# Kernel tuning notes

Hardware: AMD Instinct MI355X
Metric: run time of the kernel (lower is better)

The kernel has to match this reference:

```python
import jax, jax.numpy as jnp
import numpy as np

NEG_SLOPE = 0.01  # torch nn.LeakyReLU default


def setup_inputs() -> dict:
    key = jax.random.key(0)
    ks = jax.random.split(key, 6)
    B, L, C, D = 4, 1024, 128, 64
    return {
        "queries": jax.random.normal(ks[0], (B, L, C), dtype=jnp.float32),
        "keys": jax.random.normal(ks[1], (B, L, C), dtype=jnp.float32),
        "values": jax.random.normal(ks[2], (B, L, C), dtype=jnp.float32),
        "linear_l": jax.random.normal(ks[3], (C, D), dtype=jnp.float32) * 0.05,
        "linear_r": jax.random.normal(ks[4], (C, D), dtype=jnp.float32) * 0.05,
        "a": jax.random.normal(ks[5], (D, 1), dtype=jnp.float32) * 0.05,
    }


def reference(queries, keys, values, linear_l, linear_r, a):
    # keys/values are accepted by the torch forward but unused in its math.
    # g_l, g_r: (B, L, D)
    g_l = jnp.einsum('blc,cd->bld', queries, linear_l)
    g_r = jnp.einsum('blc,cd->bld', queries, linear_r)
    # torch repeat/repeat_interleave + view(b,l,l,-1) yields
    # g_sum[b, x, y] = g_l[b, y] + g_r[b, x]  -> (B, L, L, D)
    g_sum = g_l[:, None, :, :] + g_r[:, :, None, :]
    g_sum = jnp.where(g_sum >= 0, g_sum, NEG_SLOPE * g_sum)  # LeakyReLU
    e = jnp.einsum('bxyd,d->bxy', g_sum, a[:, 0])            # (B, L, L)
    scores = jax.nn.softmax(e, axis=-1)                       # dropout is identity in eval
    y = jnp.einsum('bxy,byd->bxd', scores, g_r)               # (B, L, D)
    return (y, scores)
```

## Files before the change

### kernel.cpp

```cpp
#include <hip/hip_runtime.h>
#include <math.h>

#define LL   1024
#define NROW 4096
#define DD   64
#define CC   128

#define C1H 0.505f
#define C2H 0.495f

typedef short    bf16x8 __attribute__((ext_vector_type(8)));
typedef float    f32x4  __attribute__((ext_vector_type(4)));
typedef _Float16 hf2    __attribute__((ext_vector_type(2)));

static __device__ __forceinline__ unsigned short bf16rne(float f) {
  unsigned u = __float_as_uint(f);
  u += 0x7fffu + ((u >> 16) & 1u);
  return (unsigned short)(u >> 16);
}

static __device__ __forceinline__ unsigned rflu(unsigned v) {
  return __builtin_amdgcn_readfirstlane(v);
}
static __device__ __forceinline__ float rflf(float v) {
  return __uint_as_float(__builtin_amdgcn_readfirstlane(__float_as_uint(v)));
}

static __device__ __forceinline__ void unpkf16(unsigned u, float& lo, float& hi) {
  union { unsigned u; hf2 h; } v; v.u = u;
  lo = (float)v.h.x;
  hi = (float)v.h.y;
}

__global__ __launch_bounds__(256) void k_proj(
    const float* __restrict__ q, const float* __restrict__ Wl,
    const float* __restrict__ Wr, const float* __restrict__ a,
    uint4* __restrict__ glg, _Float16* __restrict__ gr16,
    unsigned short* __restrict__ grTf,
    float* __restrict__ AL, float* __restrict__ AR) {
  const int bl0 = blockIdx.x * 8;
  const int b = bl0 >> 10;
  const int t = threadIdx.x;
  __shared__ __align__(16) float qs[8 * CC];
  __shared__ __align__(16) unsigned short trT[DD][8];
  __shared__ __align__(16) _Float16 trL[8][DD];

  ((float4*)qs)[t] = ((const float4*)(q + (size_t)bl0 * CC))[t];
  __syncthreads();

  const int rr = t >> 6;
  const int d  = t & 63;
  const int r0 = rr * 2, r1 = rr * 2 + 1;
  const float* q0 = qs + r0 * CC;
  const float* q1 = qs + r1 * CC;

  float aL0 = 0, aL1 = 0, aR0 = 0, aR1 = 0;
  float bL0 = 0, bL1 = 0, bR0 = 0, bR1 = 0;
#pragma unroll 8
  for (int c = 0; c < CC; c += 2) {
    float wl0 = Wl[c * DD + d],       wr0 = Wr[c * DD + d];
    float wl1 = Wl[(c + 1) * DD + d], wr1 = Wr[(c + 1) * DD + d];
    aL0 = fmaf(q0[c], wl0, aL0);  bL0 = fmaf(q0[c + 1], wl1, bL0);
    aL1 = fmaf(q1[c], wl0, aL1);  bL1 = fmaf(q1[c + 1], wl1, bL1);
    aR0 = fmaf(q0[c], wr0, aR0);  bR0 = fmaf(q0[c + 1], wr1, bR0);
    aR1 = fmaf(q1[c], wr0, aR1);  bR1 = fmaf(q1[c + 1], wr1, bR1);
  }
  float gL0 = aL0 + bL0, gL1 = aL1 + bL1;
  float gR0 = aR0 + bR0, gR1 = aR1 + bR1;

  trL[r0][d] = (_Float16)gL0;
  trL[r1][d] = (_Float16)gL1;
  gr16[(size_t)(bl0 + r0) * DD + d] = (_Float16)gR0;
  gr16[(size_t)(bl0 + r1) * DD + d] = (_Float16)gR1;
  trT[d][r0] = bf16rne(gR0);
  trT[d][r1] = bf16rne(gR1);

  float av = a[d];
  float vL0 = av * gL0, vL1 = av * gL1, vR0 = av * gR0, vR1 = av * gR1;
#pragma unroll
  for (int off = 1; off < 64; off <<= 1) {
    vL0 += __shfl_xor(vL0, off, 64);
    vL1 += __shfl_xor(vL1, off, 64);
    vR0 += __shfl_xor(vR0, off, 64);
    vR1 += __shfl_xor(vR1, off, 64);
  }
  if (d == 0) {
    AL[bl0 + r0] = vL0; AL[bl0 + r1] = vL1;
    AR[bl0 + r0] = vR0; AR[bl0 + r1] = vR1;
  }
  __syncthreads();
  if (t < 64) {
    const int kc = (bl0 & 1023) >> 5;
    const int hi = ((bl0 & 1023) >> 3) & 3;
    ((uint4*)grTf)[((size_t)((b * 32 + kc) * 4 + (t >> 4)) << 6) +
                   hi * 16 + (t & 15)] = *(const uint4*)&trT[t][0];
  } else if (t < 128) {
    int tt = t - 64;
    int r = tt >> 3, g = tt & 7;
    glg[(((size_t)(b * 8 + g)) << 10) + (bl0 & 1023) + r] =
        *(const uint4*)&trL[r][g * 8];
  }
}

__global__ __launch_bounds__(512, 4) void k_fused(
    const uint4* __restrict__ glg, const _Float16* __restrict__ gr16,
    const unsigned short* __restrict__ grTf,
    const float* __restrict__ AL, const float* __restrict__ AR,
    const float* __restrict__ a,
    float* __restrict__ scores, float* __restrict__ yout) {
  const int bl0 = blockIdx.x * 8;
  const int b = bl0 >> 10;
  const int t = threadIdx.x;
  const int w = t >> 6, l = t & 63;

  __shared__ __align__(16) float grL32[8 * DD];
  __shared__ __align__(16) unsigned short eb[8704];
  __shared__ __align__(16) float sPV[8][4][8][17];
  __shared__ __align__(16) float sSx[8][8];

  uint4 gv[4][2][2];
#pragma unroll
  for (int dblk = 0; dblk < 4; ++dblk)
#pragma unroll
    for (int yc = 0; yc < 2; ++yc)
#pragma unroll
      for (int g2 = 0; g2 < 2; ++g2)
        gv[dblk][yc][g2] =
            glg[(((size_t)(b * 8 + dblk * 2 + g2)) << 10) + yc * 512 + t];

  if (t < 256) {
    unsigned u = ((const unsigned*)(gr16 + (size_t)bl0 * DD))[t];
    float lo, hi;
    unpkf16(u, lo, hi);
    grL32[t * 2]     = lo;
    grL32[t * 2 + 1] = hi;
  }

  float sa[64];
#pragma unroll
  for (int k = 0; k < 16; ++k) {
    float4 av = *(const float4*)&a[k * 4];
    sa[k * 4 + 0] = rflf(av.x);
    sa[k * 4 + 1] = rflf(av.y);
    sa[k * 4 + 2] = rflf(av.z);
    sa[k * 4 + 3] = rflf(av.w);
  }

  float pr[8];
#pragma unroll
  for (int x = 0; x < 8; ++x) pr[x] = C1H * rflf(AR[bl0 + x]);

  float alv[2];
  alv[0] = AL[b * LL + t];
  alv[1] = AL[b * LL + 512 + t];

  float pacc[8][2];
#pragma unroll
  for (int x = 0; x < 8; ++x) { pacc[x][0] = 0.f; pacc[x][1] = 0.f; }

  __syncthreads();

  const float4* grL4 = (const float4*)grL32;
#pragma unroll
  for (int dblk = 0; dblk < 4; ++dblk) {
    float gl32[2][16];
#pragma unroll
    for (int yc = 0; yc < 2; ++yc) {
      unpkf16(gv[dblk][yc][0].x, gl32[yc][0],  gl32[yc][1]);
      unpkf16(gv[dblk][yc][0].y, gl32[yc][2],  gl32[yc][3]);
      unpkf16(gv[dblk][yc][0].z, gl32[yc][4],  gl32[yc][5]);
      unpkf16(gv[dblk][yc][0].w, gl32[yc][6],  gl32[yc][7]);
      unpkf16(gv[dblk][yc][1].x, gl32[yc][8],  gl32[yc][9]);
      unpkf16(gv[dblk][yc][1].y, gl32[yc][10], gl32[yc][11]);
      unpkf16(gv[dblk][yc][1].z, gl32[yc][12], gl32[yc][13]);
      unpkf16(gv[dblk][yc][1].w, gl32[yc][14], gl32[yc][15]);
    }
#pragma unroll
    for (int x = 0; x < 8; ++x) {
      float4 g0 = grL4[x * 16 + dblk * 4 + 0];
      float4 g1 = grL4[x * 16 + dblk * 4 + 1];
      float4 g2 = grL4[x * 16 + dblk * 4 + 2];
      float4 g3 = grL4[x * 16 + dblk * 4 + 3];
#pragma unroll
      for (int yc = 0; yc < 2; ++yc) {
        const float* gl = gl32[yc];
        float s = pacc[x][yc];
        s = fmaf(fabsf(gl[0]  + g0.x), sa[dblk * 16 + 0],  s);
        s = fmaf(fabsf(gl[1]  + g0.y), sa[dblk * 16 + 1],  s);
        s = fmaf(fabsf(gl[2]  + g0.z), sa[dblk * 16 + 2],  s);
        s = fmaf(fabsf(gl[3]  + g0.w), sa[dblk * 16 + 3],  s);
        s = fmaf(fabsf(gl[4]  + g1.x), sa[dblk * 16 + 4],  s);
        s = fmaf(fabsf(gl[5]  + g1.y), sa[dblk * 16 + 5],  s);
        s = fmaf(fabsf(gl[6]  + g1.z), sa[dblk * 16 + 6],  s);
        s = fmaf(fabsf(gl[7]  + g1.w), sa[dblk * 16 + 7],  s);
        s = fmaf(fabsf(gl[8]  + g2.x), sa[dblk * 16 + 8],  s);
        s = fmaf(fabsf(gl[9]  + g2.y), sa[dblk * 16 + 9],  s);
        s = fmaf(fabsf(gl[10] + g2.z), sa[dblk * 16 + 10], s);
        s = fmaf(fabsf(gl[11] + g2.w), sa[dblk * 16 + 11], s);
        s = fmaf(fabsf(gl[12] + g3.x), sa[dblk * 16 + 12], s);
        s = fmaf(fabsf(gl[13] + g3.y), sa[dblk * 16 + 13], s);
        s = fmaf(fabsf(gl[14] + g3.z), sa[dblk * 16 + 14], s);
        s = fmaf(fabsf(gl[15] + g3.w), sa[dblk * 16 + 15], s);
        pacc[x][yc] = s;
      }
    }
  }

  float ev[8][2], lsum[8];
#pragma unroll
  for (int x = 0; x < 8; ++x) {
    ev[x][0] = __expf(fmaf(C2H, pacc[x][0], pr[x] + C1H * alv[0]));
    ev[x][1] = __expf(fmaf(C2H, pacc[x][1], pr[x] + C1H * alv[1]));
    lsum[x] = ev[x][0] + ev[x][1];
  }
#pragma unroll
  for (int off = 1; off < 64; off <<= 1) {
#pragma unroll
    for (int x = 0; x < 8; ++x) lsum[x] += __shfl_xor(lsum[x], off, 64);
  }
  if (l == 0) {
#pragma unroll
    for (int x = 0; x < 8; ++x) sSx[x][w] = lsum[x];
  }
  __syncthreads();

  float isv[8];
#pragma unroll
  for (int x = 0; x < 8; ++x) {
    float4 s0 = *(const float4*)&sSx[x][0];
    float4 s1 = *(const float4*)&sSx[x][4];
    isv[x] = 1.0f / (((s0.x + s0.y) + (s0.z + s0.w)) +
                     ((s1.x + s1.y) + (s1.z + s1.w)));
  }

  float pv_[8][2];
#pragma unroll
  for (int yc = 0; yc < 2; ++yc) {
    int y = yc * 512 + t;
    int kc = y >> 5, k32 = t & 31;
#pragma unroll
    for (int x = 0; x < 8; ++x) {
      float p = ev[x][yc] * isv[x];
      pv_[x][yc] = p;
      eb[kc * 256 + x * 32 + k32] = bf16rne(p);
    }
  }
  __syncthreads();

  f32x4 acc[4] = {{0.f, 0.f, 0.f, 0.f}, {0.f, 0.f, 0.f, 0.f},
                  {0.f, 0.f, 0.f, 0.f}, {0.f, 0.f, 0.f, 0.f}};
  const int row16 = l & 15, hh = l >> 4;
#pragma unroll
  for (int kk = 0; kk < 4; ++kk) {
    int kc = w * 4 + kk;
    bf16x8 af = *(const bf16x8*)&eb[kc * 256 + row16 * 32 + hh * 8];
#pragma unroll
    for (int nt = 0; nt < 4; ++nt) {
      bf16x8 bfv = *(const bf16x8*)(grTf +
          ((((size_t)((b * 32 + kc) * 4 + nt)) << 6) + l) * 8);
      acc[nt] = __builtin_amdgcn_mfma_f32_16x16x32_bf16(af, bfv, acc[nt], 0, 0, 0);
    }
  }
  if (l < 32) {
#pragma unroll
    for (int nt = 0; nt < 4; ++nt)
#pragma unroll
      for (int i = 0; i < 4; ++i)
        sPV[w][nt][hh * 4 + i][row16] = acc[nt][i];
  }
  __syncthreads();
  {
    int x = t >> 6, dcol = t & 63, nt = dcol >> 4, col = dcol & 15;
    float r = 0.f;
#pragma unroll
    for (int ww = 0; ww < 8; ++ww) r += sPV[ww][nt][x][col];
    yout[(size_t)(bl0 + x) * DD + dcol] = r;
  }

#pragma unroll
  for (int yc = 0; yc < 2; ++yc) {
    int y = yc * 512 + t;
#pragma unroll
    for (int x = 0; x < 8; ++x)
      __builtin_nontemporal_store(pv_[x][yc],
                                  &scores[((size_t)(bl0 + x) << 10) + y]);
  }
}

extern "C" void kernel_launch(void* const* d_in, const int* in_sizes, int n_in,
                              void* d_out, int out_size, void* d_ws, size_t ws_size,
                              hipStream_t stream) {
  const float* q  = (const float*)d_in[0];
  const float* Wl = (const float*)d_in[3];
  const float* Wr = (const float*)d_in[4];
  const float* a  = (const float*)d_in[5];

  float* yout = (float*)d_out;
  float* esc  = yout + NROW * DD;

  float* ws = (float*)d_ws;
  float* AL = ws;
  float* AR = AL + NROW;
  uint4* glg = (uint4*)(AR + NROW);
  _Float16* gr16 = (_Float16*)(glg + (size_t)NROW * 8);
  unsigned short* grTf = (unsigned short*)(gr16 + (size_t)NROW * DD);

  k_proj <<<NROW / 8, 256, 0, stream>>>(q, Wl, Wr, a, glg, gr16, grTf, AL, AR);
  k_fused<<<NROW / 8, 512, 0, stream>>>(glg, gr16, grTf, AL, AR, a, esc, yout);
}
```

Baseline: 32.77 us.

## Halve fused kernel block size, give each thread four key columns

The fused scores kernel now runs 256 threads per block instead of 512. Each thread handles four key columns instead of two, and each wave does eight MFMA k-chunks instead of four. The gl loads move from a prefetch at kernel start into the per-d-block loop, and the score stores are issued as soon as the probabilities are computed, so the pv_ register array goes away. This amortises the broadcast loads of the query-row data and the softmax reduction over more work per thread, and halves the cross-wave partial sums. In exchange it uses more registers per thread, has fewer waves to hide latency, and loses the early load prefetch.

```diff
diff --git a/kernel.cpp b/kernel.cpp
--- a/kernel.cpp
+++ b/kernel.cpp
@@ -19,9 +19,6 @@
   return (unsigned short)(u >> 16);
 }
 
-static __device__ __forceinline__ unsigned rflu(unsigned v) {
-  return __builtin_amdgcn_readfirstlane(v);
-}
 static __device__ __forceinline__ float rflf(float v) {
   return __uint_as_float(__builtin_amdgcn_readfirstlane(__float_as_uint(v)));
 }
@@ -102,7 +99,7 @@
   }
 }
 
-__global__ __launch_bounds__(512, 4) void k_fused(
+__global__ __launch_bounds__(256, 4) void k_fused(
     const uint4* __restrict__ glg, const _Float16* __restrict__ gr16,
     const unsigned short* __restrict__ grTf,
     const float* __restrict__ AL, const float* __restrict__ AR,
@@ -115,20 +112,10 @@
 
   __shared__ __align__(16) float grL32[8 * DD];
   __shared__ __align__(16) unsigned short eb[8704];
-  __shared__ __align__(16) float sPV[8][4][8][17];
-  __shared__ __align__(16) float sSx[8][8];
-
-  uint4 gv[4][2][2];
-#pragma unroll
-  for (int dblk = 0; dblk < 4; ++dblk)
-#pragma unroll
-    for (int yc = 0; yc < 2; ++yc)
-#pragma unroll
-      for (int g2 = 0; g2 < 2; ++g2)
-        gv[dblk][yc][g2] =
-            glg[(((size_t)(b * 8 + dblk * 2 + g2)) << 10) + yc * 512 + t];
-
-  if (t < 256) {
+  __shared__ __align__(16) float sPV[4][4][8][17];
+  __shared__ __align__(16) float sSx[8][4];
+
+  {
     unsigned u = ((const unsigned*)(gr16 + (size_t)bl0 * DD))[t];
     float lo, hi;
     unpkf16(u, lo, hi);
@@ -150,30 +137,34 @@
 #pragma unroll
   for (int x = 0; x < 8; ++x) pr[x] = C1H * rflf(AR[bl0 + x]);
 
-  float alv[2];
-  alv[0] = AL[b * LL + t];
-  alv[1] = AL[b * LL + 512 + t];
-
-  float pacc[8][2];
-#pragma unroll
-  for (int x = 0; x < 8; ++x) { pacc[x][0] = 0.f; pacc[x][1] = 0.f; }
+  float alv[4];
+#pragma unroll
+  for (int yc = 0; yc < 4; ++yc) alv[yc] = AL[b * LL + yc * 256 + t];
+
+  float pacc[8][4];
+#pragma unroll
+  for (int x = 0; x < 8; ++x)
+#pragma unroll
+    for (int yc = 0; yc < 4; ++yc) pacc[x][yc] = 0.f;
 
   __syncthreads();
 
   const float4* grL4 = (const float4*)grL32;
 #pragma unroll
   for (int dblk = 0; dblk < 4; ++dblk) {
-    float gl32[2][16];
-#pragma unroll
-    for (int yc = 0; yc < 2; ++yc) {
-      unpkf16(gv[dblk][yc][0].x, gl32[yc][0],  gl32[yc][1]);
-      unpkf16(gv[dblk][yc][0].y, gl32[yc][2],  gl32[yc][3]);
-      unpkf16(gv[dblk][yc][0].z, gl32[yc][4],  gl32[yc][5]);
-      unpkf16(gv[dblk][yc][0].w, gl32[yc][6],  gl32[yc][7]);
-      unpkf16(gv[dblk][yc][1].x, gl32[yc][8],  gl32[yc][9]);
-      unpkf16(gv[dblk][yc][1].y, gl32[yc][10], gl32[yc][11]);
-      unpkf16(gv[dblk][yc][1].z, gl32[yc][12], gl32[yc][13]);
-      unpkf16(gv[dblk][yc][1].w, gl32[yc][14], gl32[yc][15]);
+    float gl32[4][16];
+#pragma unroll
+    for (int yc = 0; yc < 4; ++yc) {
+      uint4 g0 = glg[(((size_t)(b * 8 + dblk * 2 + 0)) << 10) + yc * 256 + t];
+      uint4 g1 = glg[(((size_t)(b * 8 + dblk * 2 + 1)) << 10) + yc * 256 + t];
+      unpkf16(g0.x, gl32[yc][0],  gl32[yc][1]);
+      unpkf16(g0.y, gl32[yc][2],  gl32[yc][3]);
+      unpkf16(g0.z, gl32[yc][4],  gl32[yc][5]);
+      unpkf16(g0.w, gl32[yc][6],  gl32[yc][7]);
+      unpkf16(g1.x, gl32[yc][8],  gl32[yc][9]);
+      unpkf16(g1.y, gl32[yc][10], gl32[yc][11]);
+      unpkf16(g1.z, gl32[yc][12], gl32[yc][13]);
+      unpkf16(g1.w, gl32[yc][14], gl32[yc][15]);
     }
 #pragma unroll
     for (int x = 0; x < 8; ++x) {
@@ -182,7 +173,7 @@
       float4 g2 = grL4[x * 16 + dblk * 4 + 2];
       float4 g3 = grL4[x * 16 + dblk * 4 + 3];
 #pragma unroll
-      for (int yc = 0; yc < 2; ++yc) {
+      for (int yc = 0; yc < 4; ++yc) {
         const float* gl = gl32[yc];
         float s = pacc[x][yc];
         s = fmaf(fabsf(gl[0]  + g0.x), sa[dblk * 16 + 0],  s);
@@ -206,12 +197,15 @@
     }
   }
 
-  float ev[8][2], lsum[8];
+  float ev[8][4], lsum[8];
 #pragma unroll
   for (int x = 0; x < 8; ++x) {
-    ev[x][0] = __expf(fmaf(C2H, pacc[x][0], pr[x] + C1H * alv[0]));
-    ev[x][1] = __expf(fmaf(C2H, pacc[x][1], pr[x] + C1H * alv[1]));
-    lsum[x] = ev[x][0] + ev[x][1];
+    lsum[x] = 0.f;
+#pragma unroll
+    for (int yc = 0; yc < 4; ++yc) {
+      ev[x][yc] = __expf(fmaf(C2H, pacc[x][yc], pr[x] + C1H * alv[yc]));
+      lsum[x] += ev[x][yc];
+    }
   }
 #pragma unroll
   for (int off = 1; off < 64; off <<= 1) {
@@ -228,20 +222,17 @@
 #pragma unroll
   for (int x = 0; x < 8; ++x) {
     float4 s0 = *(const float4*)&sSx[x][0];
-    float4 s1 = *(const float4*)&sSx[x][4];
-    isv[x] = 1.0f / (((s0.x + s0.y) + (s0.z + s0.w)) +
-                     ((s1.x + s1.y) + (s1.z + s1.w)));
-  }
-
-  float pv_[8][2];
-#pragma unroll
-  for (int yc = 0; yc < 2; ++yc) {
-    int y = yc * 512 + t;
+    isv[x] = 1.0f / ((s0.x + s0.y) + (s0.z + s0.w));
+  }
+
+#pragma unroll
+  for (int yc = 0; yc < 4; ++yc) {
+    int y = yc * 256 + t;
     int kc = y >> 5, k32 = t & 31;
 #pragma unroll
     for (int x = 0; x < 8; ++x) {
       float p = ev[x][yc] * isv[x];
-      pv_[x][yc] = p;
+      __builtin_nontemporal_store(p, &scores[((size_t)(bl0 + x) << 10) + y]);
       eb[kc * 256 + x * 32 + k32] = bf16rne(p);
     }
   }
@@ -251,8 +242,8 @@
                   {0.f, 0.f, 0.f, 0.f}, {0.f, 0.f, 0.f, 0.f}};
   const int row16 = l & 15, hh = l >> 4;
 #pragma unroll
-  for (int kk = 0; kk < 4; ++kk) {
-    int kc = w * 4 + kk;
+  for (int kk = 0; kk < 8; ++kk) {
+    int kc = w * 8 + kk;
     bf16x8 af = *(const bf16x8*)&eb[kc * 256 + row16 * 32 + hh * 8];
 #pragma unroll
     for (int nt = 0; nt < 4; ++nt) {
@@ -269,21 +260,14 @@
         sPV[w][nt][hh * 4 + i][row16] = acc[nt][i];
   }
   __syncthreads();
-  {
-    int x = t >> 6, dcol = t & 63, nt = dcol >> 4, col = dcol & 15;
+#pragma unroll
+  for (int rep = 0; rep < 2; ++rep) {
+    int o = t + rep * 256;
+    int x = o >> 6, dcol = o & 63, nt = dcol >> 4, col = dcol & 15;
     float r = 0.f;
 #pragma unroll
-    for (int ww = 0; ww < 8; ++ww) r += sPV[ww][nt][x][col];
+    for (int ww = 0; ww < 4; ++ww) r += sPV[ww][nt][x][col];
     yout[(size_t)(bl0 + x) * DD + dcol] = r;
-  }
-
-#pragma unroll
-  for (int yc = 0; yc < 2; ++yc) {
-    int y = yc * 512 + t;
-#pragma unroll
-    for (int x = 0; x < 8; ++x)
-      __builtin_nontemporal_store(pv_[x][yc],
-                                  &scores[((size_t)(bl0 + x) << 10) + y]);
   }
 }
 
@@ -306,5 +290,5 @@
   unsigned short* grTf = (unsigned short*)(gr16 + (size_t)NROW * DD);
 
   k_proj <<<NROW / 8, 256, 0, stream>>>(q, Wl, Wr, a, glg, gr16, grTf, AL, AR);
-  k_fused<<<NROW / 8, 512, 0, stream>>>(glg, gr16, grTf, AL, AR, a, esc, yout);
-}
+  k_fused<<<NROW / 8, 256, 0, stream>>>(glg, gr16, grTf, AL, AR, a, esc, yout);
+}
```

New measurement: 36.78 us. 1.12x slower.

## Split fused softmax kernel into score kernel and separate PV matmul kernel

Applied to the files above, without the earlier changes.

The fused kernel is split in two. The first kernel computes the softmax scores, writes them to global memory and also stores a bf16 copy to a workspace buffer. The second kernel reads that buffer and runs the MFMA product with g_r to produce y. This drops the LDS staging buffer and a barrier from the scores kernel, which may raise occupancy. In exchange it adds an extra kernel launch and a global write plus read of about 8 MB of bf16 probabilities.

```diff
diff --git a/kernel.cpp b/kernel.cpp
--- a/kernel.cpp
+++ b/kernel.cpp
@@ -19,9 +19,6 @@
   return (unsigned short)(u >> 16);
 }
 
-static __device__ __forceinline__ unsigned rflu(unsigned v) {
-  return __builtin_amdgcn_readfirstlane(v);
-}
 static __device__ __forceinline__ float rflf(float v) {
   return __uint_as_float(__builtin_amdgcn_readfirstlane(__float_as_uint(v)));
 }
@@ -102,20 +99,17 @@
   }
 }
 
-__global__ __launch_bounds__(512, 4) void k_fused(
+__global__ __launch_bounds__(512, 4) void k_e(
     const uint4* __restrict__ glg, const _Float16* __restrict__ gr16,
-    const unsigned short* __restrict__ grTf,
     const float* __restrict__ AL, const float* __restrict__ AR,
     const float* __restrict__ a,
-    float* __restrict__ scores, float* __restrict__ yout) {
+    float* __restrict__ scores, unsigned short* __restrict__ ebg) {
   const int bl0 = blockIdx.x * 8;
   const int b = bl0 >> 10;
   const int t = threadIdx.x;
   const int w = t >> 6, l = t & 63;
 
   __shared__ __align__(16) float grL32[8 * DD];
-  __shared__ __align__(16) unsigned short eb[8704];
-  __shared__ __align__(16) float sPV[8][4][8][17];
   __shared__ __align__(16) float sSx[8][8];
 
   uint4 gv[4][2][2];
@@ -233,7 +227,7 @@
                      ((s1.x + s1.y) + (s1.z + s1.w)));
   }
 
-  float pv_[8][2];
+  const size_t eb0 = (size_t)blockIdx.x * 8192;
 #pragma unroll
   for (int yc = 0; yc < 2; ++yc) {
     int y = yc * 512 + t;
@@ -241,19 +235,31 @@
 #pragma unroll
     for (int x = 0; x < 8; ++x) {
       float p = ev[x][yc] * isv[x];
-      pv_[x][yc] = p;
-      eb[kc * 256 + x * 32 + k32] = bf16rne(p);
+      __builtin_nontemporal_store(p, &scores[((size_t)(bl0 + x) << 10) + y]);
+      __builtin_nontemporal_store(bf16rne(p), &ebg[eb0 + kc * 256 + x * 32 + k32]);
     }
   }
-  __syncthreads();
+}
+
+__global__ __launch_bounds__(512, 4) void k_pv(
+    const unsigned short* __restrict__ ebg,
+    const unsigned short* __restrict__ grTf,
+    float* __restrict__ yout) {
+  const int bl0 = blockIdx.x * 8;
+  const int b = bl0 >> 10;
+  const int t = threadIdx.x;
+  const int w = t >> 6, l = t & 63;
+
+  __shared__ __align__(16) float sPV[8][4][8][17];
 
   f32x4 acc[4] = {{0.f, 0.f, 0.f, 0.f}, {0.f, 0.f, 0.f, 0.f},
                   {0.f, 0.f, 0.f, 0.f}, {0.f, 0.f, 0.f, 0.f}};
   const int row16 = l & 15, hh = l >> 4;
+  const size_t eb0 = (size_t)blockIdx.x * 8192;
 #pragma unroll
   for (int kk = 0; kk < 4; ++kk) {
     int kc = w * 4 + kk;
-    bf16x8 af = *(const bf16x8*)&eb[kc * 256 + row16 * 32 + hh * 8];
+    bf16x8 af = *(const bf16x8*)&ebg[eb0 + kc * 256 + row16 * 32 + hh * 8];
 #pragma unroll
     for (int nt = 0; nt < 4; ++nt) {
       bf16x8 bfv = *(const bf16x8*)(grTf +
@@ -275,15 +281,6 @@
 #pragma unroll
     for (int ww = 0; ww < 8; ++ww) r += sPV[ww][nt][x][col];
     yout[(size_t)(bl0 + x) * DD + dcol] = r;
-  }
-
-#pragma unroll
-  for (int yc = 0; yc < 2; ++yc) {
-    int y = yc * 512 + t;
-#pragma unroll
-    for (int x = 0; x < 8; ++x)
-      __builtin_nontemporal_store(pv_[x][yc],
-                                  &scores[((size_t)(bl0 + x) << 10) + y]);
   }
 }
 
@@ -304,7 +301,9 @@
   uint4* glg = (uint4*)(AR + NROW);
   _Float16* gr16 = (_Float16*)(glg + (size_t)NROW * 8);
   unsigned short* grTf = (unsigned short*)(gr16 + (size_t)NROW * DD);
-
-  k_proj <<<NROW / 8, 256, 0, stream>>>(q, Wl, Wr, a, glg, gr16, grTf, AL, AR);
-  k_fused<<<NROW / 8, 512, 0, stream>>>(glg, gr16, grTf, AL, AR, a, esc, yout);
-}
+  unsigned short* ebg = grTf + (size_t)NROW * LL / 4;
+
+  k_proj<<<NROW / 8, 256, 0, stream>>>(q, Wl, Wr, a, glg, gr16, grTf, AL, AR);
+  k_e   <<<NROW / 8, 512, 0, stream>>>(glg, gr16, AL, AR, a, esc, ebg);
+  k_pv  <<<NROW / 8, 512, 0, stream>>>(ebg, grTf, yout);
+}
```

Measured after the change: 35.92 us. 9.6% more time.
